# Kernel optimization log

Hardware: AMD Instinct MI355X
Metric: run time of the kernel (lower is better)

## Reference

```python
import jax, jax.numpy as jnp
import numpy as np

SCALE = 1.0
LOG_SCALE = float(np.log(SCALE))
HALF_LOG_2PI = float(0.5 * np.log(2.0 * np.pi))


def setup_inputs() -> dict:
    key = jax.random.key(0)
    k1, k2, k3 = jax.random.split(key, 3)
    data = jax.random.normal(k1, (128, 128, 64), dtype=jnp.float32)      # b n d
    targets = jax.random.normal(k2, (128, 128), dtype=jnp.float32)       # b n
    W = jax.random.normal(k3, (64, 4096), dtype=jnp.float32)             # d t (task_pool.squeeze().T)
    return {"data": data, "targets": targets, "W": W}


def reference(data, targets, W):
    # err[b,n,t] = y_bn - x_bn . w_t
    err = targets[..., None] - jnp.einsum('bnd,dt->bnt', data, W)
    # Normal(0, scale).log_prob
    logp = -0.5 * (err / SCALE) ** 2 - LOG_SCALE - HALF_LOG_2PI
    # prefix-sum of log-probs over points: csum[:, i-1] == alpha at step i
    csum = jnp.cumsum(logp, axis=1)                       # b n t
    alpha = jax.nn.softmax(csum[:, :-1], axis=-1)         # b (n-1) t
    w_mmse = jnp.einsum('bnt,dt->bnd', alpha, W)          # b (n-1) d
    preds_rest = jnp.einsum('bnd,bnd->bn', data[:, 1:], w_mmse)
    pred0 = data[:, 0] @ W.mean(axis=1)                   # prior-mean prediction
    return jnp.concatenate([pred0[:, None], preds_rest], axis=1)  # b n
```

## Files before the change

kernel.cpp:

```cpp
#include <hip/hip_runtime.h>


#define B 128
#define N 128
#define D 64
#define T 4096
#define NT 16
#define NTILES (N / NT)
#define NCHUNK 16
#define K1_BLK 256
#define K1_WPB (K1_BLK / 64)
#define K1_GRID (B * NCHUNK / K1_WPB)

#define DPP_XOR1 0xB1
#define DPP_XOR2 0x4E
#define DPP_XOR4 0x141
#define DPP_XOR8 0x140

template <int CTRL>
__device__ __forceinline__ float dppf(float x) {
    return __int_as_float(
        __builtin_amdgcn_mov_dpp(__float_as_int(x), CTRL, 0xF, 0xF, true));
}

__device__ __forceinline__ float dpp_max16(float m) {
    m = fmaxf(m, dppf<DPP_XOR1>(m));
    m = fmaxf(m, dppf<DPP_XOR2>(m));
    m = fmaxf(m, dppf<DPP_XOR4>(m));
    m = fmaxf(m, dppf<DPP_XOR8>(m));
    return m;
}

__device__ __forceinline__ float dpp_sum16(float s) {
    s += dppf<DPP_XOR1>(s);
    s += dppf<DPP_XOR2>(s);
    s += dppf<DPP_XOR4>(s);
    s += dppf<DPP_XOR8>(s);
    return s;
}

__global__ __launch_bounds__(K1_BLK, 2)
void dmmse_k1(const float* __restrict__ data,
              const float* __restrict__ targets,
              const float* __restrict__ W,
              float4* __restrict__ part)
{
    const int tid   = threadIdx.x;
    const int lane  = tid & 63;
    const int g     = blockIdx.x * K1_WPB + (tid >> 6);
    const int b     = g >> 4;
    const int chunk = g & 15;

    const float4* W4   = reinterpret_cast<const float4*>(W);
    const int     wcol = chunk * 64 + lane;

    float csum0 = 0.f, csum1 = 0.f, csum2 = 0.f, csum3 = 0.f;
    float Mg = 0.f;

    for (int j = 0; j < NTILES; ++j) {
        float mu[NT][4];
        #pragma unroll
        for (int i = 0; i < NT; ++i) { mu[i][0]=0.f; mu[i][1]=0.f; mu[i][2]=0.f; mu[i][3]=0.f; }

        const float* drow = data + (b * N + j * NT) * D;

#define FMA_GROUP(dc_, wv0, wv1, wv2, wv3)                                     \
        _Pragma("unroll")                                                      \
        for (int i = 0; i < NT; ++i) {                                         \
            const float4 x = *reinterpret_cast<const float4*>(drow + i * D + (dc_)); \
            mu[i][0] = fmaf(x.x, wv0.x, mu[i][0]);                             \
            mu[i][1] = fmaf(x.x, wv0.y, mu[i][1]);                             \
            mu[i][2] = fmaf(x.x, wv0.z, mu[i][2]);                             \
            mu[i][3] = fmaf(x.x, wv0.w, mu[i][3]);                             \
            mu[i][0] = fmaf(x.y, wv1.x, mu[i][0]);                             \
            mu[i][1] = fmaf(x.y, wv1.y, mu[i][1]);                             \
            mu[i][2] = fmaf(x.y, wv1.z, mu[i][2]);                             \
            mu[i][3] = fmaf(x.y, wv1.w, mu[i][3]);                             \
            mu[i][0] = fmaf(x.z, wv2.x, mu[i][0]);                             \
            mu[i][1] = fmaf(x.z, wv2.y, mu[i][1]);                             \
            mu[i][2] = fmaf(x.z, wv2.z, mu[i][2]);                             \
            mu[i][3] = fmaf(x.z, wv2.w, mu[i][3]);                             \
            mu[i][0] = fmaf(x.w, wv3.x, mu[i][0]);                             \
            mu[i][1] = fmaf(x.w, wv3.y, mu[i][1]);                             \
            mu[i][2] = fmaf(x.w, wv3.z, mu[i][2]);                             \
            mu[i][3] = fmaf(x.w, wv3.w, mu[i][3]);                             \
        }

        float4 a0 = W4[0 * (T / 4) + wcol];
        float4 a1 = W4[1 * (T / 4) + wcol];
        float4 a2 = W4[2 * (T / 4) + wcol];
        float4 a3 = W4[3 * (T / 4) + wcol];
        for (int dc = 0; dc < D - 4; dc += 4) {
            const float4 b0 = W4[(dc + 4) * (T / 4) + wcol];
            const float4 b1 = W4[(dc + 5) * (T / 4) + wcol];
            const float4 b2 = W4[(dc + 6) * (T / 4) + wcol];
            const float4 b3 = W4[(dc + 7) * (T / 4) + wcol];
            FMA_GROUP(dc, a0, a1, a2, a3)
            a0 = b0; a1 = b1; a2 = b2; a3 = b3;
        }
        FMA_GROUP(D - 4, a0, a1, a2, a3)
#undef FMA_GROUP

        #pragma unroll
        for (int i = 0; i < NT; ++i) {
            const int n = j * NT + i;

            const float e0 = __expf(csum0 - Mg);
            const float e1 = __expf(csum1 - Mg);
            const float e2 = __expf(csum2 - Mg);
            const float e3 = __expf(csum3 - Mg);
            float s = (e0 + e1) + (e2 + e3);
            float p = fmaf(e0, mu[i][0],
                      fmaf(e1, mu[i][1],
                      fmaf(e2, mu[i][2], e3 * mu[i][3])));

            s = dpp_sum16(s);
            p = dpp_sum16(p);

            float mw = Mg, sw = s, pw = p;
            {
                const float mx = __shfl_xor(mw, 16, 64);
                const float sx = __shfl_xor(sw, 16, 64);
                const float px = __shfl_xor(pw, 16, 64);
                const float mn = fmaxf(mw, mx);
                const float fa = __expf(mw - mn);
                const float fb = __expf(mx - mn);
                sw = fmaf(sw, fa, sx * fb);
                pw = fmaf(pw, fa, px * fb);
                mw = mn;
            }
            {
                const float mx = __shfl_xor(mw, 32, 64);
                const float sx = __shfl_xor(sw, 32, 64);
                const float px = __shfl_xor(pw, 32, 64);
                const float mn = fmaxf(mw, mx);
                const float fa = __expf(mw - mn);
                const float fb = __expf(mx - mn);
                sw = fmaf(sw, fa, sx * fb);
                pw = fmaf(pw, fa, px * fb);
                mw = mn;
            }
            if (lane == 0)
                part[chunk * (B * N) + b * N + n] = make_float4(mw, sw, pw, 0.f);

            if (n < N - 1) {
                const float y = targets[b * N + n];
                float e;
                e = y - mu[i][0]; csum0 = fmaf(-0.5f * e, e, csum0);
                e = y - mu[i][1]; csum1 = fmaf(-0.5f * e, e, csum1);
                e = y - mu[i][2]; csum2 = fmaf(-0.5f * e, e, csum2);
                e = y - mu[i][3]; csum3 = fmaf(-0.5f * e, e, csum3);
            }
            Mg = dpp_max16(fmaxf(fmaxf(csum0, csum1), fmaxf(csum2, csum3)));
        }
    }
}

__global__ __launch_bounds__(256)
void dmmse_k2(const float4* __restrict__ part,
              float* __restrict__ out)
{
    const int t = blockIdx.x * 256 + threadIdx.x;

    float M = -__builtin_inff(), S = 0.f, P = 0.f;
    #pragma unroll
    for (int c = 0; c < NCHUNK; ++c) {
        const float4 v = part[c * (B * N) + t];
        const float nM = fmaxf(M, v.x);
        const float aa = __expf(M - nM);
        const float f  = __expf(v.x - nM);
        S = S * aa + v.y * f;
        P = P * aa + v.z * f;
        M = nM;
    }
    out[t] = P / S;
}

extern "C" void kernel_launch(void* const* d_in, const int* in_sizes, int n_in,
                              void* d_out, int out_size, void* d_ws, size_t ws_size,
                              hipStream_t stream)
{
    const float* data    = (const float*)d_in[0];
    const float* targets = (const float*)d_in[1];
    const float* W       = (const float*)d_in[2];
    float* out           = (float*)d_out;
    float4* part         = (float4*)d_ws;

    dmmse_k1<<<K1_GRID, K1_BLK, 0, stream>>>(data, targets, W, part);
    dmmse_k2<<<(B * N) / 256, 256, 0, stream>>>(part, out);
}
```

Before: 245.9 us.

## Split k1 into producer matmul wave and consumer softmax wave via LDS

```diff
diff --git a/kernel.cpp b/kernel.cpp
--- a/kernel.cpp
+++ b/kernel.cpp
@@ -5,12 +5,10 @@
 #define N 128
 #define D 64
 #define T 4096
-#define NT 16
+#define NT 8
 #define NTILES (N / NT)
 #define NCHUNK 16
-#define K1_BLK 256
-#define K1_WPB (K1_BLK / 64)
-#define K1_GRID (B * NCHUNK / K1_WPB)
+#define K1_GRID (B * NCHUNK)
 
 #define DPP_XOR1 0xB1
 #define DPP_XOR2 0x4E
@@ -39,7 +37,7 @@
     return s;
 }
 
-__global__ __launch_bounds__(K1_BLK, 2)
+__global__ __launch_bounds__(128, 2)
 void dmmse_k1(const float* __restrict__ data,
               const float* __restrict__ targets,
               const float* __restrict__ W,
@@ -47,9 +45,11 @@
 {
     const int tid   = threadIdx.x;
     const int lane  = tid & 63;
-    const int g     = blockIdx.x * K1_WPB + (tid >> 6);
-    const int b     = g >> 4;
-    const int chunk = g & 15;
+    const int wid   = tid >> 6;
+    const int b     = blockIdx.x >> 4;
+    const int chunk = blockIdx.x & 15;
+
+    __shared__ float muf[2][NT][256];
 
     const float4* W4   = reinterpret_cast<const float4*>(W);
     const int     wcol = chunk * 64 + lane;
@@ -57,102 +57,117 @@
     float csum0 = 0.f, csum1 = 0.f, csum2 = 0.f, csum3 = 0.f;
     float Mg = 0.f;
 
-    for (int j = 0; j < NTILES; ++j) {
-        float mu[NT][4];
-        #pragma unroll
-        for (int i = 0; i < NT; ++i) { mu[i][0]=0.f; mu[i][1]=0.f; mu[i][2]=0.f; mu[i][3]=0.f; }
-
-        const float* drow = data + (b * N + j * NT) * D;
+    for (int k = 0; k <= NTILES; ++k) {
+        if (wid == 0 && k < NTILES) {
+            float mu[NT][4];
+            #pragma unroll
+            for (int i = 0; i < NT; ++i) { mu[i][0]=0.f; mu[i][1]=0.f; mu[i][2]=0.f; mu[i][3]=0.f; }
+
+            const float* drow = data + (b * N + k * NT) * D;
 
 #define FMA_GROUP(dc_, wv0, wv1, wv2, wv3)                                     \
-        _Pragma("unroll")                                                      \
-        for (int i = 0; i < NT; ++i) {                                         \
-            const float4 x = *reinterpret_cast<const float4*>(drow + i * D + (dc_)); \
-            mu[i][0] = fmaf(x.x, wv0.x, mu[i][0]);                             \
-            mu[i][1] = fmaf(x.x, wv0.y, mu[i][1]);                             \
-            mu[i][2] = fmaf(x.x, wv0.z, mu[i][2]);                             \
-            mu[i][3] = fmaf(x.x, wv0.w, mu[i][3]);                             \
-            mu[i][0] = fmaf(x.y, wv1.x, mu[i][0]);                             \
-            mu[i][1] = fmaf(x.y, wv1.y, mu[i][1]);                             \
-            mu[i][2] = fmaf(x.y, wv1.z, mu[i][2]);                             \
-            mu[i][3] = fmaf(x.y, wv1.w, mu[i][3]);                             \
-            mu[i][0] = fmaf(x.z, wv2.x, mu[i][0]);                             \
-            mu[i][1] = fmaf(x.z, wv2.y, mu[i][1]);                             \
-            mu[i][2] = fmaf(x.z, wv2.z, mu[i][2]);                             \
-            mu[i][3] = fmaf(x.z, wv2.w, mu[i][3]);                             \
-            mu[i][0] = fmaf(x.w, wv3.x, mu[i][0]);                             \
-            mu[i][1] = fmaf(x.w, wv3.y, mu[i][1]);                             \
-            mu[i][2] = fmaf(x.w, wv3.z, mu[i][2]);                             \
-            mu[i][3] = fmaf(x.w, wv3.w, mu[i][3]);                             \
+            _Pragma("unroll")                                                  \
+            for (int i = 0; i < NT; ++i) {                                     \
+                const float4 x = *reinterpret_cast<const float4*>(drow + i * D + (dc_)); \
+                mu[i][0] = fmaf(x.x, wv0.x, mu[i][0]);                         \
+                mu[i][1] = fmaf(x.x, wv0.y, mu[i][1]);                         \
+                mu[i][2] = fmaf(x.x, wv0.z, mu[i][2]);                         \
+                mu[i][3] = fmaf(x.x, wv0.w, mu[i][3]);                         \
+                mu[i][0] = fmaf(x.y, wv1.x, mu[i][0]);                         \
+                mu[i][1] = fmaf(x.y, wv1.y, mu[i][1]);                         \
+                mu[i][2] = fmaf(x.y, wv1.z, mu[i][2]);                         \
+                mu[i][3] = fmaf(x.y, wv1.w, mu[i][3]);                         \
+                mu[i][0] = fmaf(x.z, wv2.x, mu[i][0]);                         \
+                mu[i][1] = fmaf(x.z, wv2.y, mu[i][1]);                         \
+                mu[i][2] = fmaf(x.z, wv2.z, mu[i][2]);                         \
+                mu[i][3] = fmaf(x.z, wv2.w, mu[i][3]);                         \
+                mu[i][0] = fmaf(x.w, wv3.x, mu[i][0]);                         \
+                mu[i][1] = fmaf(x.w, wv3.y, mu[i][1]);                         \
+                mu[i][2] = fmaf(x.w, wv3.z, mu[i][2]);                         \
+                mu[i][3] = fmaf(x.w, wv3.w, mu[i][3]);                         \
+            }
+
+            float4 a0 = W4[0 * (T / 4) + wcol];
+            float4 a1 = W4[1 * (T / 4) + wcol];
+            float4 a2 = W4[2 * (T / 4) + wcol];
+            float4 a3 = W4[3 * (T / 4) + wcol];
+            for (int dc = 0; dc < D - 4; dc += 4) {
+                const float4 b0 = W4[(dc + 4) * (T / 4) + wcol];
+                const float4 b1 = W4[(dc + 5) * (T / 4) + wcol];
+                const float4 b2 = W4[(dc + 6) * (T / 4) + wcol];
+                const float4 b3 = W4[(dc + 7) * (T / 4) + wcol];
+                FMA_GROUP(dc, a0, a1, a2, a3)
+                a0 = b0; a1 = b1; a2 = b2; a3 = b3;
+            }
+            FMA_GROUP(D - 4, a0, a1, a2, a3)
+#undef FMA_GROUP
+
+            #pragma unroll
+            for (int i = 0; i < NT; ++i)
+                *reinterpret_cast<float4*>(&muf[k & 1][i][lane << 2]) =
+                    make_float4(mu[i][0], mu[i][1], mu[i][2], mu[i][3]);
         }
 
-        float4 a0 = W4[0 * (T / 4) + wcol];
-        float4 a1 = W4[1 * (T / 4) + wcol];
-        float4 a2 = W4[2 * (T / 4) + wcol];
-        float4 a3 = W4[3 * (T / 4) + wcol];
-        for (int dc = 0; dc < D - 4; dc += 4) {
-            const float4 b0 = W4[(dc + 4) * (T / 4) + wcol];
-            const float4 b1 = W4[(dc + 5) * (T / 4) + wcol];
-            const float4 b2 = W4[(dc + 6) * (T / 4) + wcol];
-            const float4 b3 = W4[(dc + 7) * (T / 4) + wcol];
-            FMA_GROUP(dc, a0, a1, a2, a3)
-            a0 = b0; a1 = b1; a2 = b2; a3 = b3;
+        if (wid == 1 && k >= 1) {
+            const int t = k - 1;
+            #pragma unroll
+            for (int i = 0; i < NT; ++i) {
+                const int n = t * NT + i;
+
+                const float4 mu4 =
+                    *reinterpret_cast<const float4*>(&muf[t & 1][i][lane << 2]);
+
+                const float e0 = __expf(csum0 - Mg);
+                const float e1 = __expf(csum1 - Mg);
+                const float e2 = __expf(csum2 - Mg);
+                const float e3 = __expf(csum3 - Mg);
+                float s = (e0 + e1) + (e2 + e3);
+                float p = fmaf(e0, mu4.x,
+                          fmaf(e1, mu4.y,
+                          fmaf(e2, mu4.z, e3 * mu4.w)));
+
+                s = dpp_sum16(s);
+                p = dpp_sum16(p);
+
+                float mw = Mg, sw = s, pw = p;
+                {
+                    const float mx = __shfl_xor(mw, 16, 64);
+                    const float sx = __shfl_xor(sw, 16, 64);
+                    const float px = __shfl_xor(pw, 16, 64);
+                    const float mn = fmaxf(mw, mx);
+                    const float fa = __expf(mw - mn);
+                    const float fb = __expf(mx - mn);
+                    sw = fmaf(sw, fa, sx * fb);
+                    pw = fmaf(pw, fa, px * fb);
+                    mw = mn;
+                }
+                {
+                    const float mx = __shfl_xor(mw, 32, 64);
+                    const float sx = __shfl_xor(sw, 32, 64);
+                    const float px = __shfl_xor(pw, 32, 64);
+                    const float mn = fmaxf(mw, mx);
+                    const float fa = __expf(mw - mn);
+                    const float fb = __expf(mx - mn);
+                    sw = fmaf(sw, fa, sx * fb);
+                    pw = fmaf(pw, fa, px * fb);
+                    mw = mn;
+                }
+                if (lane == 0)
+                    part[chunk * (B * N) + b * N + n] = make_float4(mw, sw, pw, 0.f);
+
+                if (n < N - 1) {
+                    const float y = targets[b * N + n];
+                    float e;
+                    e = y - mu4.x; csum0 = fmaf(-0.5f * e, e, csum0);
+                    e = y - mu4.y; csum1 = fmaf(-0.5f * e, e, csum1);
+                    e = y - mu4.z; csum2 = fmaf(-0.5f * e, e, csum2);
+                    e = y - mu4.w; csum3 = fmaf(-0.5f * e, e, csum3);
+                }
+                Mg = dpp_max16(fmaxf(fmaxf(csum0, csum1), fmaxf(csum2, csum3)));
+            }
         }
-        FMA_GROUP(D - 4, a0, a1, a2, a3)
-#undef FMA_GROUP
-
-        #pragma unroll
-        for (int i = 0; i < NT; ++i) {
-            const int n = j * NT + i;
-
-            const float e0 = __expf(csum0 - Mg);
-            const float e1 = __expf(csum1 - Mg);
-            const float e2 = __expf(csum2 - Mg);
-            const float e3 = __expf(csum3 - Mg);
-            float s = (e0 + e1) + (e2 + e3);
-            float p = fmaf(e0, mu[i][0],
-                      fmaf(e1, mu[i][1],
-                      fmaf(e2, mu[i][2], e3 * mu[i][3])));
-
-            s = dpp_sum16(s);
-            p = dpp_sum16(p);
-
-            float mw = Mg, sw = s, pw = p;
-            {
-                const float mx = __shfl_xor(mw, 16, 64);
-                const float sx = __shfl_xor(sw, 16, 64);
-                const float px = __shfl_xor(pw, 16, 64);
-                const float mn = fmaxf(mw, mx);
-                const float fa = __expf(mw - mn);
-                const float fb = __expf(mx - mn);
-                sw = fmaf(sw, fa, sx * fb);
-                pw = fmaf(pw, fa, px * fb);
-                mw = mn;
-            }
-            {
-                const float mx = __shfl_xor(mw, 32, 64);
-                const float sx = __shfl_xor(sw, 32, 64);
-                const float px = __shfl_xor(pw, 32, 64);
-                const float mn = fmaxf(mw, mx);
-                const float fa = __expf(mw - mn);
-                const float fb = __expf(mx - mn);
-                sw = fmaf(sw, fa, sx * fb);
-                pw = fmaf(pw, fa, px * fb);
-                mw = mn;
-            }
-            if (lane == 0)
-                part[chunk * (B * N) + b * N + n] = make_float4(mw, sw, pw, 0.f);
-
-            if (n < N - 1) {
-                const float y = targets[b * N + n];
-                float e;
-                e = y - mu[i][0]; csum0 = fmaf(-0.5f * e, e, csum0);
-                e = y - mu[i][1]; csum1 = fmaf(-0.5f * e, e, csum1);
-                e = y - mu[i][2]; csum2 = fmaf(-0.5f * e, e, csum2);
-                e = y - mu[i][3]; csum3 = fmaf(-0.5f * e, e, csum3);
-            }
-            Mg = dpp_max16(fmaxf(fmaxf(csum0, csum1), fmaxf(csum2, csum3)));
-        }
+
+        __syncthreads();
     }
 }
 
@@ -186,6 +201,6 @@
     float* out           = (float*)d_out;
     float4* part         = (float4*)d_ws;
 
-    dmmse_k1<<<K1_GRID, K1_BLK, 0, stream>>>(data, targets, W, part);
+    dmmse_k1<<<K1_GRID, 128, 0, stream>>>(data, targets, W, part);
     dmmse_k2<<<(B * N) / 256, 256, 0, stream>>>(part, out);
 }
```

Result: slower. 254.0 us (+3.3%).
